# Kernel tuning notes

Hardware: AMD Instinct MI355X
Metric: run time of the kernel (lower is better)

## Reference

```python
import jax, jax.numpy as jnp
import numpy as np

GAMMA = 0.6
EPS = 1e-10
T = 20
ALPHA = 2.0
BETA = 1.5
LAM = 2.0
ETA = 10.0
PLACEHOLDER = -1
ENABLE_BONUS = False

B, K, V = 64, 8, 50257


def _nan_to(x, val):
    # torch.nan_to_num(nan=val) replaces only NaN, keeps +-inf
    return jnp.where(jnp.isnan(x), jnp.asarray(val, x.dtype), x)


def _costeer(llm, base, steer):
    # llm/base/steer: [B, V]
    llm_log = jax.nn.log_softmax(_nan_to(llm, -100.0), axis=-1)
    base_log = jax.nn.log_softmax(_nan_to(base, -100.0), axis=-1)
    steer_log = jax.nn.log_softmax(_nan_to(steer, -100.0), axis=-1)
    delta = steer_log - base_log
    delta = jnp.where(jnp.isnan(delta), jnp.zeros((), delta.dtype), delta)

    def body(t, carry):
        q_sum, log_p, prev = carry
        q_sum = q_sum + ALPHA * (log_p - llm_log) + BETA * delta
        t_f = t.astype(llm_log.dtype)
        denom = t_f * LAM + 1.0 / ETA
        lp = (t_f * LAM * llm_log + q_sum + prev / ETA) / denom
        lp = jax.nn.log_softmax(lp, axis=-1)
        return (q_sum, lp, lp)

    q0 = jnp.zeros_like(llm_log)
    _, log_p, _ = jax.lax.fori_loop(1, T + 1, body, (q0, llm_log, llm_log))
    return log_p


def setup_inputs() -> dict:
    key = jax.random.key(0)
    k1, k2, k3, k4, k5, k6 = jax.random.split(key, 6)
    target_logits = jax.random.normal(k1, (B * K, V), dtype=jnp.float32)
    base_logits = jax.random.normal(k2, (B * K, V), dtype=jnp.float32)
    steer_logits = jax.random.normal(k3, (B * K, V), dtype=jnp.float32)
    draft_token_ids = jax.random.randint(k4, (B, K), 0, V, dtype=jnp.int32)
    num_draft_tokens = jax.random.randint(k5, (B,), 1, K + 1, dtype=jnp.int32)
    bonus_token_ids = jax.random.randint(k6, (B,), 0, V, dtype=jnp.int32)
    return {
        "target_logits": target_logits,
        "base_logits": base_logits,
        "steer_logits": steer_logits,
        "draft_token_ids": draft_token_ids,
        "num_draft_tokens": num_draft_tokens,
        "bonus_token_ids": bonus_token_ids,
    }


def reference(target_logits, base_logits, steer_logits, draft_token_ids,
              num_draft_tokens, bonus_token_ids):
    tl = target_logits.reshape(B, K, V)
    bl = base_logits.reshape(B, K, V)
    sl = steer_logits.reshape(B, K, V)

    target_probs = jax.nn.softmax(tl, axis=-1)
    base_probs = jax.nn.softmax(bl, axis=-1)

    idx = draft_token_ids[..., None]  # [B, K, 1]
    p_llm = jnp.take_along_axis(target_probs, idx, axis=-1)[..., 0]  # [B, K]
    p_base = jnp.take_along_axis(base_probs, idx, axis=-1)[..., 0]

    pos = jnp.arange(K, dtype=jnp.int32)[None, :]           # [1, K]
    valid = pos < num_draft_tokens[:, None]                  # [B, K]
    accept = (p_llm > GAMMA * (p_base + EPS)) & valid
    prefix = jnp.cumprod(accept.astype(jnp.int32), axis=1)   # 1 until first reject
    cnt = prefix.sum(axis=1).astype(jnp.int32)               # accepted count [B]
    rejected = cnt < num_draft_tokens                        # [B]

    # gather the (first-rejected) row per request; clamp for fully-accepted reqs
    rp = jnp.minimum(cnt, K - 1)[:, None, None]              # [B,1,1]
    llm_r = jnp.take_along_axis(tl, rp, axis=1)[:, 0]        # [B, V]
    base_r = jnp.take_along_axis(bl, rp, axis=1)[:, 0]
    steer_r = jnp.take_along_axis(sl, rp, axis=1)[:, 0]

    fused = _costeer(llm_r, base_r, steer_r)                 # [B, V]
    recovered = jnp.argmax(fused, axis=-1).astype(jnp.int32)  # [B]

    ph = jnp.full((B, K), PLACEHOLDER, dtype=jnp.int32)
    out_main = jnp.where(pos < cnt[:, None], draft_token_ids,
                         jnp.where((pos == cnt[:, None]) & rejected[:, None],
                                   recovered[:, None], ph))  # [B, K]

    if ENABLE_BONUS:
        bonus_col = jnp.where(~rejected, bonus_token_ids,
                              jnp.full((B,), PLACEHOLDER, jnp.int32))[:, None]
    else:
        bonus_col = jnp.full((B, 1), PLACEHOLDER, dtype=jnp.int32)
    output_token_ids = jnp.concatenate([out_main, bonus_col], axis=1)  # [B, K+1]

    return output_token_ids, cnt, fused
```

## Files before the change

### kernel.cpp

```cpp
#include <hip/hip_runtime.h>
#include <cstdint>
#include <cstddef>

#define VDIM 50257
#define BNUM 64
#define KNUM 8
#define TITER 20

#define SEGA   12564
#define NSEGA  4
#define SEGF   1572
#define NSEGF  32
#define EPTF   7
#define SEGS   6284
#define NSEGS  8

__device__ __forceinline__ void upd(float& m, float& s, float x) {
    float d = m - x;
    float e = __expf(-fabsf(d));
    float t1 = (d >= 0.0f) ? 1.0f : e;
    float t2 = (d >= 0.0f) ? e : 1.0f;
    s = fmaf(s, t1, t2);
    m = fmaxf(m, x);
}

__device__ __forceinline__ void comb(float& m, float& s, float mo, float so) {
    float mn = fmaxf(m, mo);
    s = s * __expf(m - mn) + so * __expf(mo - mn);
    m = mn;
}

__device__ __forceinline__ void blockReduceMS(float& m, float& s, float* shm, int tid) {
    int lane = tid & 63, wid = tid >> 6;
    #pragma unroll
    for (int off = 32; off > 0; off >>= 1) {
        float mo = __shfl_down(m, off);
        float so = __shfl_down(s, off);
        comb(m, s, mo, so);
    }
    if (lane == 0) { shm[2 * wid] = m; shm[2 * wid + 1] = s; }
    __syncthreads();
    if (tid == 0) {
        float M = shm[0], S = shm[1];
        #pragma unroll
        for (int w = 1; w < 4; w++) comb(M, S, shm[2 * w], shm[2 * w + 1]);
        shm[0] = M; shm[1] = S;
    }
    __syncthreads();
    m = shm[0]; s = shm[1];
    __syncthreads();
}

__device__ __forceinline__ void blockReduceArgmax(float& v, int& idx, float* shmf, int* shmi, int tid) {
    int lane = tid & 63, wid = tid >> 6;
    #pragma unroll
    for (int off = 32; off > 0; off >>= 1) {
        float vo = __shfl_down(v, off);
        int   io = __shfl_down(idx, off);
        if (vo > v || (vo == v && io < idx)) { v = vo; idx = io; }
    }
    if (lane == 0) { shmf[wid] = v; shmi[wid] = idx; }
    __syncthreads();
    if (tid == 0) {
        #pragma unroll
        for (int w = 1; w < 4; w++)
            if (shmf[w] > v || (shmf[w] == v && shmi[w] < idx)) { v = shmf[w]; idx = shmi[w]; }
        shmf[0] = v; shmi[0] = idx;
    }
    __syncthreads();
    v = shmf[0]; idx = shmi[0];
    __syncthreads();
}

__global__ __launch_bounds__(256) void k_stats(
        const float* __restrict__ tgt, const float* __restrict__ bse,
        const int* __restrict__ ndraft,
        float* __restrict__ pm_a, float* __restrict__ ps_a) {
    int bid  = blockIdx.x;
    int task = bid >> 2, seg = bid & 3;
    int which = task >> 9, r = task & 511;
    if ((r & 7) >= ndraft[r >> 3]) return;

    const float* row = (which ? bse : tgt) + (size_t)r * VDIM;
    int start = seg * SEGA;
    int len = VDIM - start; if (len > SEGA) len = SEGA;
    const float* p = row + start;
    int tid = threadIdx.x;

    float m0 = -3.0e38f, m1 = -3.0e38f, m2 = -3.0e38f, m3 = -3.0e38f;
    float s0 = 0.f, s1 = 0.f, s2 = 0.f, s3 = 0.f;

    int mis  = (int)(((uintptr_t)p & 15) >> 2);
    int head = (4 - mis) & 3;
    if (tid < head) upd(m0, s0, p[tid]);
    const float4* v4 = (const float4*)(p + head);
    int n4 = (len - head) >> 2;
    for (int g = tid; g < n4; g += 256) {
        float4 x = v4[g];
        upd(m0, s0, x.x); upd(m1, s1, x.y); upd(m2, s2, x.z); upd(m3, s3, x.w);
    }
    int j = head + (n4 << 2) + tid;
    if (j < len) upd(m0, s0, p[j]);

    comb(m0, s0, m1, s1);
    comb(m2, s2, m3, s3);
    comb(m0, s0, m2, s2);

    __shared__ float shm[16];
    blockReduceMS(m0, s0, shm, tid);
    if (tid == 0) { pm_a[bid] = m0; ps_a[bid] = s0; }
}

__global__ __launch_bounds__(256) void k_fused(
        const float* __restrict__ tgt, const float* __restrict__ bse,
        const float* __restrict__ str,
        const int* __restrict__ draft, const int* __restrict__ ndraft,
        const float* __restrict__ pm_a, const float* __restrict__ ps_a,
        float aa, float bb,
        float* __restrict__ out_tok, float* __restrict__ out_cnt,
        float* __restrict__ out_fused, int* __restrict__ rci,
        float* __restrict__ pmf, float* __restrict__ psf,
        float* __restrict__ pvf, int* __restrict__ pif) {
    int blk = blockIdx.x;
    int b = blk >> 5, seg = blk & (NSEGF - 1);
    int tid = threadIdx.x;

    __shared__ float shp[16];
    __shared__ float shm[16];
    __shared__ int   shmi[8];
    __shared__ int   sh_rp;

    int nd = ndraft[b];

    if (tid < 16) {
        int which = tid >> 3, k = tid & 7, r = b * KNUM + k;
        float pval = 0.0f;
        if (k < nd) {
            float M = -3.0e38f, S = 0.0f;
            int base = (which * 512 + r) * NSEGA;
            #pragma unroll
            for (int sg = 0; sg < NSEGA; sg++) comb(M, S, pm_a[base + sg], ps_a[base + sg]);
            float lse = M + __logf(S);
            const float* row = (which ? bse : tgt) + (size_t)r * VDIM;
            pval = __expf(row[draft[r]] - lse);
        }
        shp[tid] = pval;
    }
    __syncthreads();
    if (tid == 0) {
        int cnt = 0; bool chain = true;
        #pragma unroll
        for (int kk = 0; kk < KNUM; kk++) {
            float pl = shp[kk], pb = shp[8 + kk];
            bool acc = (kk < nd) && (pl > 0.6f * (pb + 1e-10f));
            chain = chain && acc;
            if (chain) cnt++;
        }
        int rej = (cnt < nd) ? 1 : 0;
        int rp  = cnt < (KNUM - 1) ? cnt : (KNUM - 1);
        sh_rp = rp;
        if (seg == 0) {
            #pragma unroll
            for (int kk = 0; kk < KNUM; kk++)
                out_tok[b * (KNUM + 1) + kk] = (kk < cnt) ? (float)draft[b * KNUM + kk] : -1.0f;
            out_tok[b * (KNUM + 1) + KNUM] = -1.0f;
            out_cnt[b] = (float)cnt;
            rci[b] = rp; rci[64 + b] = cnt; rci[128 + b] = rej;
        }
    }
    __syncthreads();
    int rp = sh_rp;

    size_t roff = (size_t)(b * KNUM + rp) * VDIM;
    const float* tl = tgt + roff;
    const float* bl = bse + roff;
    const float* sl = str + roff;

    int start = seg * SEGF;
    int len = VDIM - start; if (len > SEGF) len = SEGF;
    float* dst = out_fused + (size_t)b * VDIM + start;

    float m = -3.0e38f, s = 0.0f, bv = -3.0e38f;
    int bi = 0x7fffffff;
    #pragma unroll
    for (int i = 0; i < EPTF; i++) {
        int j = tid + i * 256;
        if (j < len) {
            int g = start + j;
            float y = fmaf(aa, tl[g], bb * (sl[g] - bl[g]));
            dst[j] = y;
            upd(m, s, y);
            if (y > bv) { bv = y; bi = g; }
        }
    }
    blockReduceMS(m, s, shm, tid);
    blockReduceArgmax(bv, bi, shm, shmi, tid);
    if (tid == 0) { pmf[blk] = m; psf[blk] = s; pvf[blk] = bv; pif[blk] = bi; }
}

__global__ __launch_bounds__(256) void k_sub(
        const int* __restrict__ rci,
        const float* __restrict__ pmf, const float* __restrict__ psf,
        const float* __restrict__ pvf, const int* __restrict__ pif,
        float* __restrict__ out_tok, float* __restrict__ out_fused) {
    int blk = blockIdx.x;
    int b = blk >> 3, seg = blk & (NSEGS - 1);
    int tid = threadIdx.x;

    __shared__ float shZ;
    __shared__ int   shG;

    if (tid < 64) {
        float M = -3.0e38f, S = 0.0f, V = -3.0e38f;
        int I = 0x7fffffff;
        if (tid < NSEGF) {
            int idx = b * NSEGF + tid;
            M = pmf[idx]; S = psf[idx]; V = pvf[idx]; I = pif[idx];
        }
        #pragma unroll
        for (int off = 16; off > 0; off >>= 1) {
            float Mo = __shfl_down(M, off);
            float So = __shfl_down(S, off);
            float Vo = __shfl_down(V, off);
            int   Io = __shfl_down(I, off);
            comb(M, S, Mo, So);
            if (Vo > V || (Vo == V && Io < I)) { V = Vo; I = Io; }
        }
        if (tid == 0) { shZ = M + __logf(S); shG = I; }
    }
    __syncthreads();
    float Z = shZ;

    int start = seg * SEGS;
    int len = VDIM - start; if (len > SEGS) len = SEGS;
    float* p = out_fused + (size_t)b * VDIM + start;

    int mis  = (int)(((uintptr_t)p & 15) >> 2);
    int head = (4 - mis) & 3;
    if (head > len) head = len;
    if (tid < head) p[tid] -= Z;
    float4* v4 = (float4*)(p + head);
    int n4 = (len - head) >> 2;
    for (int g = tid; g < n4; g += 256) {
        float4 x = v4[g];
        x.x -= Z; x.y -= Z; x.z -= Z; x.w -= Z;
        v4[g] = x;
    }
    int j = head + (n4 << 2) + tid;
    if (j < len) p[j] -= Z;

    if (seg == 0 && tid == 0 && rci[128 + b]) {
        out_tok[b * (KNUM + 1) + rci[64 + b]] = (float)shG;
    }
}


extern "C" void kernel_launch(void* const* d_in, const int* in_sizes, int n_in,
                              void* d_out, int out_size, void* d_ws, size_t ws_size,
                              hipStream_t stream) {
    const float* tgt   = (const float*)d_in[0];
    const float* bse   = (const float*)d_in[1];
    const float* str   = (const float*)d_in[2];
    const int*   draft = (const int*)d_in[3];
    const int*   nd    = (const int*)d_in[4];

    float* out       = (float*)d_out;
    float* out_tok   = out;
    float* out_cnt   = out + BNUM * (KNUM + 1);
    float* out_fused = out + BNUM * (KNUM + 1) + BNUM;

    float* wsf  = (float*)d_ws;
    float* pm_a = wsf;
    float* ps_a = wsf + 4096;
    float* pmf  = wsf + 8192;
    float* psf  = wsf + 10240;
    float* pvf  = wsf + 12288;
    int*   wsi  = (int*)(wsf + 14336);
    int*   rci  = wsi;
    int*   pif  = wsi + 192;

    float dd = 0.0f, ee = 0.0f, aa = 1.0f, bb = 0.0f;
    for (int t = 1; t <= TITER; t++) {
        dd += 2.0f * (aa - 1.0f);
        ee += 2.0f * bb + 1.5f;
        float tf = (float)t;
        float denom = tf * 2.0f + 0.1f;
        float an = (tf * 2.0f + dd + aa * 0.1f) / denom;
        float bn = (ee + bb * 0.1f) / denom;
        aa = an; bb = bn;
    }

    hipLaunchKernelGGL(k_stats, dim3(1024 * NSEGA), dim3(256), 0, stream,
                       tgt, bse, nd, pm_a, ps_a);
    hipLaunchKernelGGL(k_fused, dim3(BNUM * NSEGF), dim3(256), 0, stream,
                       tgt, bse, str, draft, nd, pm_a, ps_a, aa, bb,
                       out_tok, out_cnt, out_fused, rci, pmf, psf, pvf, pif);
    hipLaunchKernelGGL(k_sub, dim3(BNUM * NSEGS), dim3(256), 0, stream,
                       rci, pmf, psf, pvf, pif, out_tok, out_fused);
}
```

Baseline: 269.0 us.

## Fuse normalization pass into fused kernel via per-row grid spin barrier

Merges the separate subtract-logsumexp kernel into the fused-logit kernel. Each row's 8 segment blocks publish partial max/sum/argmax, increment a per-row flag counter and spin until all peers arrive, then write normalized values straight from registers with nontemporal stores. This removes one kernel launch and the read-modify-write pass over the [64,V] output. The cost is fewer blocks (512) with 25 elements per thread held in registers. It also relies on all blocks of a row being co-resident, which 512 blocks at 2 per CU should satisfy.

Result: slower. 281.3 us (+4.6%).

```diff
diff --git a/kernel.cpp b/kernel.cpp
--- a/kernel.cpp
+++ b/kernel.cpp
@@ -9,11 +9,9 @@
 
 #define SEGA   12564
 #define NSEGA  4
-#define SEGF   1572
-#define NSEGF  32
-#define EPTF   7
-#define SEGS   6284
-#define NSEGS  8
+#define SEGF   6284
+#define NSEGF  8
+#define EPTF   25
 
 __device__ __forceinline__ void upd(float& m, float& s, float x) {
     float d = m - x;
@@ -75,8 +73,12 @@
 __global__ __launch_bounds__(256) void k_stats(
         const float* __restrict__ tgt, const float* __restrict__ bse,
         const int* __restrict__ ndraft,
-        float* __restrict__ pm_a, float* __restrict__ ps_a) {
+        float* __restrict__ pm_a, float* __restrict__ ps_a,
+        unsigned int* __restrict__ flags) {
     int bid  = blockIdx.x;
+    int tid  = threadIdx.x;
+    if (bid == 0 && tid < BNUM) flags[tid] = 0u;
+
     int task = bid >> 2, seg = bid & 3;
     int which = task >> 9, r = task & 511;
     if ((r & 7) >= ndraft[r >> 3]) return;
@@ -85,7 +87,6 @@
     int start = seg * SEGA;
     int len = VDIM - start; if (len > SEGA) len = SEGA;
     const float* p = row + start;
-    int tid = threadIdx.x;
 
     float m0 = -3.0e38f, m1 = -3.0e38f, m2 = -3.0e38f, m3 = -3.0e38f;
     float s0 = 0.f, s1 = 0.f, s2 = 0.f, s3 = 0.f;
@@ -111,24 +112,26 @@
     if (tid == 0) { pm_a[bid] = m0; ps_a[bid] = s0; }
 }
 
-__global__ __launch_bounds__(256) void k_fused(
+__global__ __launch_bounds__(256, 2) void k_fused(
         const float* __restrict__ tgt, const float* __restrict__ bse,
         const float* __restrict__ str,
         const int* __restrict__ draft, const int* __restrict__ ndraft,
         const float* __restrict__ pm_a, const float* __restrict__ ps_a,
         float aa, float bb,
         float* __restrict__ out_tok, float* __restrict__ out_cnt,
-        float* __restrict__ out_fused, int* __restrict__ rci,
-        float* __restrict__ pmf, float* __restrict__ psf,
-        float* __restrict__ pvf, int* __restrict__ pif) {
+        float* __restrict__ out_fused,
+        float* pmf, float* psf, float* pvf, int* pif,
+        unsigned int* flags) {
     int blk = blockIdx.x;
-    int b = blk >> 5, seg = blk & (NSEGF - 1);
+    int b = blk >> 3, seg = blk & (NSEGF - 1);
     int tid = threadIdx.x;
 
     __shared__ float shp[16];
     __shared__ float shm[16];
     __shared__ int   shmi[8];
-    __shared__ int   sh_rp;
+    __shared__ int   sh_rp, sh_cnt, sh_rej;
+    __shared__ float shZ;
+    __shared__ int   shG;
 
     int nd = ndraft[b];
 
@@ -156,16 +159,15 @@
             chain = chain && acc;
             if (chain) cnt++;
         }
-        int rej = (cnt < nd) ? 1 : 0;
-        int rp  = cnt < (KNUM - 1) ? cnt : (KNUM - 1);
-        sh_rp = rp;
+        sh_rej = (cnt < nd) ? 1 : 0;
+        sh_cnt = cnt;
+        sh_rp  = cnt < (KNUM - 1) ? cnt : (KNUM - 1);
         if (seg == 0) {
             #pragma unroll
             for (int kk = 0; kk < KNUM; kk++)
                 out_tok[b * (KNUM + 1) + kk] = (kk < cnt) ? (float)draft[b * KNUM + kk] : -1.0f;
             out_tok[b * (KNUM + 1) + KNUM] = -1.0f;
             out_cnt[b] = (float)cnt;
-            rci[b] = rp; rci[64 + b] = cnt; rci[128 + b] = rej;
         }
     }
     __syncthreads();
@@ -178,47 +180,46 @@
 
     int start = seg * SEGF;
     int len = VDIM - start; if (len > SEGF) len = SEGF;
-    float* dst = out_fused + (size_t)b * VDIM + start;
-
+
+    float Y[EPTF];
     float m = -3.0e38f, s = 0.0f, bv = -3.0e38f;
     int bi = 0x7fffffff;
     #pragma unroll
     for (int i = 0; i < EPTF; i++) {
         int j = tid + i * 256;
+        float y = 0.0f;
         if (j < len) {
             int g = start + j;
-            float y = fmaf(aa, tl[g], bb * (sl[g] - bl[g]));
-            dst[j] = y;
+            y = fmaf(aa, tl[g], bb * (sl[g] - bl[g]));
             upd(m, s, y);
             if (y > bv) { bv = y; bi = g; }
         }
+        Y[i] = y;
     }
     blockReduceMS(m, s, shm, tid);
     blockReduceArgmax(bv, bi, shm, shmi, tid);
-    if (tid == 0) { pmf[blk] = m; psf[blk] = s; pvf[blk] = bv; pif[blk] = bi; }
-}
-
-__global__ __launch_bounds__(256) void k_sub(
-        const int* __restrict__ rci,
-        const float* __restrict__ pmf, const float* __restrict__ psf,
-        const float* __restrict__ pvf, const int* __restrict__ pif,
-        float* __restrict__ out_tok, float* __restrict__ out_fused) {
-    int blk = blockIdx.x;
-    int b = blk >> 3, seg = blk & (NSEGS - 1);
-    int tid = threadIdx.x;
-
-    __shared__ float shZ;
-    __shared__ int   shG;
-
-    if (tid < 64) {
-        float M = -3.0e38f, S = 0.0f, V = -3.0e38f;
-        int I = 0x7fffffff;
-        if (tid < NSEGF) {
-            int idx = b * NSEGF + tid;
-            M = pmf[idx]; S = psf[idx]; V = pvf[idx]; I = pif[idx];
-        }
-        #pragma unroll
-        for (int off = 16; off > 0; off >>= 1) {
+
+    if (tid == 0) {
+        atomicExch(&pmf[blk], m);
+        atomicExch(&psf[blk], s);
+        atomicExch(&pvf[blk], bv);
+        atomicExch(&pif[blk], bi);
+        __threadfence();
+        atomicAdd(&flags[b], 1u);
+        while (atomicAdd(&flags[b], 0u) < (unsigned)NSEGF) {
+            __builtin_amdgcn_s_sleep(2);
+        }
+    }
+    __syncthreads();
+
+    if (tid < NSEGF) {
+        int idx = b * NSEGF + tid;
+        float M = atomicAdd(&pmf[idx], 0.0f);
+        float S = atomicAdd(&psf[idx], 0.0f);
+        float V = atomicAdd(&pvf[idx], 0.0f);
+        int   I = atomicAdd(&pif[idx], 0);
+        #pragma unroll
+        for (int off = 4; off > 0; off >>= 1) {
             float Mo = __shfl_down(M, off);
             float So = __shfl_down(S, off);
             float Vo = __shfl_down(V, off);
@@ -231,26 +232,15 @@
     __syncthreads();
     float Z = shZ;
 
-    int start = seg * SEGS;
-    int len = VDIM - start; if (len > SEGS) len = SEGS;
-    float* p = out_fused + (size_t)b * VDIM + start;
-
-    int mis  = (int)(((uintptr_t)p & 15) >> 2);
-    int head = (4 - mis) & 3;
-    if (head > len) head = len;
-    if (tid < head) p[tid] -= Z;
-    float4* v4 = (float4*)(p + head);
-    int n4 = (len - head) >> 2;
-    for (int g = tid; g < n4; g += 256) {
-        float4 x = v4[g];
-        x.x -= Z; x.y -= Z; x.z -= Z; x.w -= Z;
-        v4[g] = x;
-    }
-    int j = head + (n4 << 2) + tid;
-    if (j < len) p[j] -= Z;
-
-    if (seg == 0 && tid == 0 && rci[128 + b]) {
-        out_tok[b * (KNUM + 1) + rci[64 + b]] = (float)shG;
+    float* dst = out_fused + (size_t)b * VDIM + start;
+    #pragma unroll
+    for (int i = 0; i < EPTF; i++) {
+        int j = tid + i * 256;
+        if (j < len) __builtin_nontemporal_store(Y[i] - Z, &dst[j]);
+    }
+
+    if (seg == 0 && tid == 0 && sh_rej) {
+        out_tok[b * (KNUM + 1) + sh_cnt] = (float)shG;
     }
 }
 
@@ -273,11 +263,11 @@
     float* pm_a = wsf;
     float* ps_a = wsf + 4096;
     float* pmf  = wsf + 8192;
-    float* psf  = wsf + 10240;
-    float* pvf  = wsf + 12288;
-    int*   wsi  = (int*)(wsf + 14336);
-    int*   rci  = wsi;
-    int*   pif  = wsi + 192;
+    float* psf  = wsf + 8704;
+    float* pvf  = wsf + 9216;
+    int*   wsi  = (int*)(wsf + 9728);
+    int*   pif  = wsi;
+    unsigned int* flags = (unsigned int*)(wsi + 512);
 
     float dd = 0.0f, ee = 0.0f, aa = 1.0f, bb = 0.0f;
     for (int t = 1; t <= TITER; t++) {
@@ -291,10 +281,8 @@
     }
 
     hipLaunchKernelGGL(k_stats, dim3(1024 * NSEGA), dim3(256), 0, stream,
-                       tgt, bse, nd, pm_a, ps_a);
+                       tgt, bse, nd, pm_a, ps_a, flags);
     hipLaunchKernelGGL(k_fused, dim3(BNUM * NSEGF), dim3(256), 0, stream,
                        tgt, bse, str, draft, nd, pm_a, ps_a, aa, bb,
-                       out_tok, out_cnt, out_fused, rci, pmf, psf, pvf, pif);
-    hipLaunchKernelGGL(k_sub, dim3(BNUM * NSEGS), dim3(256), 0, stream,
-                       rci, pmf, psf, pvf, pif, out_tok, out_fused);
-}
+                       out_tok, out_cnt, out_fused, pmf, psf, pvf, pif, flags);
+}
```
